# Kernel optimization log

Hardware: AMD Instinct MI355X
Metric: run time of the kernel (lower is better)

The kernel has to match this reference:

```python
import jax, jax.numpy as jnp
import numpy as np

N_BATCH, N_ATOMS = 32, 1024


def _param_tables():
    # Species ids: 0 = padding, 1 = H (Z=1), 2 = O (Z=8). Symmetric tables, pad row/col zero.
    d0 = np.zeros((3, 3), np.float32)
    p1 = np.zeros((3, 3), np.float32)
    p2 = np.zeros((3, 3), np.float32)
    d0[1, 1] = 157.5488; p1[1, 1] = -0.1661; p2[1, 1] = 6.25      # 001-001
    d0[1, 2] = d0[2, 1] = 216.7852                                 # 001-008
    p1[1, 2] = p1[2, 1] = -1.0
    p2[1, 2] = p2[2, 1] = 1.6492
    d0[2, 2] = 122.9794; p1[2, 2] = 1.0; p2[2, 2] = 0.1958         # 008-008
    return jnp.asarray(d0), jnp.asarray(p1), jnp.asarray(p2)


def setup_inputs() -> dict:
    key = jax.random.key(0)
    kz, kb = jax.random.split(key)
    # Atomic numbers in {1, 8} (H/O), the only species with params in the dict.
    zbits = jax.random.randint(kz, (N_BATCH, N_ATOMS), 0, 2)
    Z = jnp.where(zbits == 0, 1, 8).astype(jnp.int32)
    # Bond orders Pij in (0, 1); strictly positive so b**pbe2 is smooth.
    B = jax.random.uniform(kb, (N_BATCH, N_ATOMS, N_ATOMS), jnp.float32)
    d0_table, pbe1_table, pbe2_table = _param_tables()
    return {"Z": Z, "B": B, "d0_table": d0_table,
            "pbe1_table": pbe1_table, "pbe2_table": pbe2_table}


def reference(Z, B, d0_table, pbe1_table, pbe2_table):
    # Map atomic number -> table id (0 pad, 1 for Z=1, 2 for Z=8).
    zmap = jnp.zeros((9,), jnp.int32).at[1].set(1).at[8].set(2)
    idx = zmap[Z]                              # [nb, na]
    ii = idx[:, :, None]                       # species of atom i
    jj = idx[:, None, :]                       # species of atom j
    d0 = d0_table[ii, jj]                      # [nb, na, na] pairwise param gather
    p1 = pbe1_table[ii, jj]
    p2 = pbe2_table[ii, jj]
    # Original indexes B[:, jatom, iatom] for pair (i, j), i < j -> transpose.
    bij = jnp.abs(jnp.swapaxes(B, 1, 2))       # bij[b, i, j] = |B[b, j, i]|
    e_ij = -d0 * bij * jnp.exp(p1 * (1.0 - bij ** p2))
    n = Z.shape[1]
    pair_mask = jnp.triu(jnp.ones((n, n), bool), k=1)   # i < j only
    valid = pair_mask[None] & (Z[:, :, None] != 0) & (Z[:, None, :] != 0)
    E = jnp.sum(jnp.where(valid, e_ij, 0.0), axis=(1, 2))[:, None]  # [nb, 1]
    return E
```

## Files before the change

kernel.cpp:

```cpp
#include <hip/hip_runtime.h>

#define NATOMS  1024
#define NB      32
#define WPB     4
#define BLK     (WPB * 64)
#define BPBATCH 64
#define WAVES   (BPBATCH * WPB)
#define PPW     ((NATOMS / 2) / WAVES)

__global__ __launch_bounds__(BLK, 8) void reax_partial(
    const int*   __restrict__ Z,
    const float* __restrict__ B,
    const float* __restrict__ d0t,
    const float* __restrict__ p1t,
    const float* __restrict__ p2t,
    float*       __restrict__ ws)
{
    const int b    = blockIdx.y;
    const int wave = blockIdx.x * WPB + (threadIdx.x >> 6);
    const int lane = threadIdx.x & 63;

    const float LOG2E = 1.4426950408889634f;
    const float d0_0 = d0t[4], d0_1 = d0t[5], d0_2 = d0t[8];
    const float p1_0 = p1t[4], p1_1 = p1t[5], p1_2 = p1t[8];
    const float p2_0 = p2t[4], p2_1 = p2t[5], p2_2 = p2t[8];
    const float de_0 = d0_0 * __builtin_amdgcn_exp2f(p1_0 * LOG2E);
    const float de_1 = d0_1 * __builtin_amdgcn_exp2f(p1_1 * LOG2E);
    const float de_2 = d0_2 * __builtin_amdgcn_exp2f(p1_2 * LOG2E);
    const float c1_0 = -p1_0 * LOG2E, c1_1 = -p1_1 * LOG2E, c1_2 = -p1_2 * LOG2E;

    __shared__ float t_shf[NATOMS];
    const int* Zrow = Z + b * NATOMS;
    for (int i = threadIdx.x; i < NATOMS; i += BLK)
        t_shf[i] = (Zrow[i] == 8) ? 1.0f : 0.0f;
    __syncthreads();

    const float* Bb = B + (size_t)b * NATOMS * NATOMS;
    float sum0 = 0.0f, sum1 = 0.0f;

    for (int pp = 0; pp < PPW; ++pp) {
        const int p = wave + pp * WAVES;
        #pragma unroll
        for (int r = 0; r < 2; ++r) {
            const int j = r ? (NATOMS - 1 - p) : p;
            if (j == 0) continue;
            const int tj = (t_shf[j] != 0.0f);
            const float dea = tj ? de_1 : de_0, dde = tj ? (de_2 - de_1) : (de_1 - de_0);
            const float c1a = tj ? c1_1 : c1_0, dc1 = tj ? (c1_2 - c1_1) : (c1_1 - c1_0);
            const float p2a = tj ? p2_1 : p2_0, dp2 = tj ? (p2_2 - p2_1) : (p2_1 - p2_0);

            const float*  Brow  = Bb + (size_t)j * NATOMS;
            const float4* Brow4 = (const float4*)Brow;
            const float4* Trow4 = (const float4*)t_shf;
            const int nv = j >> 2;

            #define ELEM(xc, tc, acc)                                       \
            {                                                               \
                const float bb  = fabsf(xc);                                \
                const float p2  = fmaf(tc, dp2, p2a);                       \
                const float c1  = fmaf(tc, dc1, c1a);                       \
                const float de  = fmaf(tc, dde, dea);                       \
                const float lg  = __builtin_amdgcn_logf(bb);                \
                const float pw  = __builtin_amdgcn_exp2f(p2 * lg);          \
                const float ex  = __builtin_amdgcn_exp2f(fmaf(c1, pw, lg)); \
                acc = fmaf(de, ex, acc);                                    \
            }

            #pragma unroll 4
            for (int v = lane; v < nv; v += 64) {
                const float4 x  = Brow4[v];
                const float4 t4 = Trow4[v];
                ELEM(x.x, t4.x, sum0) ELEM(x.y, t4.y, sum1)
                ELEM(x.z, t4.z, sum0) ELEM(x.w, t4.w, sum1)
            }
            const int i = (nv << 2) + lane;
            if (i < j) {
                ELEM(Brow[i], t_shf[i], sum0)
            }
            #undef ELEM
        }
    }

    float sum = sum0 + sum1;
    #pragma unroll
    for (int off = 32; off; off >>= 1) sum += __shfl_down(sum, off, 64);
    if (lane == 0) ws[b * WAVES + wave] = sum;
}

__global__ __launch_bounds__(64) void reax_reduce(
    const float* __restrict__ ws, float* __restrict__ out)
{
    const int b = blockIdx.x;
    const int t = threadIdx.x;
    float s = ws[b * WAVES + t]       + ws[b * WAVES + t + 64]
            + ws[b * WAVES + t + 128] + ws[b * WAVES + t + 192];
    #pragma unroll
    for (int off = 32; off; off >>= 1) s += __shfl_down(s, off, 64);
    if (t == 0) out[b] = -s;
}

extern "C" void kernel_launch(void* const* d_in, const int* in_sizes, int n_in,
                              void* d_out, int out_size, void* d_ws, size_t ws_size,
                              hipStream_t stream) {
    const int*   Z   = (const int*)  d_in[0];
    const float* B   = (const float*)d_in[1];
    const float* d0t = (const float*)d_in[2];
    const float* p1t = (const float*)d_in[3];
    const float* p2t = (const float*)d_in[4];
    float* out = (float*)d_out;
    float* ws  = (float*)d_ws;

    dim3 grid(BPBATCH, NB);
    reax_partial<<<grid, BLK, 0, stream>>>(Z, B, d0t, p1t, p2t, ws);
    reax_reduce<<<NB, 64, 0, stream>>>(ws, out);
}
```

Measured before the change: 23.79 us.

## Fuse reduction into main kernel via atomics and register-cache species row

Removes the second reduction kernel: each block sums its wave partials in shared memory and atomically adds into the output, which is zeroed with a memset beforehand. The species flags for the whole row are loaded once into four float4 registers per lane, replacing per-iteration shared-memory loads, and the inner loop is fully unrolled into four guarded steps. It also drops the occupancy hint from launch bounds. The cost is a memset launch, float atomics with nondeterministic summation order, and higher register pressure.

```diff
diff --git a/kernel.cpp b/kernel.cpp
--- a/kernel.cpp
+++ b/kernel.cpp
@@ -8,13 +8,13 @@
 #define WAVES   (BPBATCH * WPB)
 #define PPW     ((NATOMS / 2) / WAVES)
 
-__global__ __launch_bounds__(BLK, 8) void reax_partial(
+__global__ __launch_bounds__(BLK) void reax_fused(
     const int*   __restrict__ Z,
     const float* __restrict__ B,
     const float* __restrict__ d0t,
     const float* __restrict__ p1t,
     const float* __restrict__ p2t,
-    float*       __restrict__ ws)
+    float*       __restrict__ out)
 {
     const int b    = blockIdx.y;
     const int wave = blockIdx.x * WPB + (threadIdx.x >> 6);
@@ -35,6 +35,12 @@
         t_shf[i] = (Zrow[i] == 8) ? 1.0f : 0.0f;
     __syncthreads();
 
+    const float4* Trow4 = (const float4*)t_shf;
+    const float4 tt0 = Trow4[lane];
+    const float4 tt1 = Trow4[lane + 64];
+    const float4 tt2 = Trow4[lane + 128];
+    const float4 tt3 = Trow4[lane + 192];
+
     const float* Bb = B + (size_t)b * NATOMS * NATOMS;
     float sum0 = 0.0f, sum1 = 0.0f;
 
@@ -51,7 +57,6 @@
 
             const float*  Brow  = Bb + (size_t)j * NATOMS;
             const float4* Brow4 = (const float4*)Brow;
-            const float4* Trow4 = (const float4*)t_shf;
             const int nv = j >> 2;
 
             #define ELEM(xc, tc, acc)                                       \
@@ -66,13 +71,18 @@
                 acc = fmaf(de, ex, acc);                                    \
             }
 
-            #pragma unroll 4
-            for (int v = lane; v < nv; v += 64) {
-                const float4 x  = Brow4[v];
-                const float4 t4 = Trow4[v];
-                ELEM(x.x, t4.x, sum0) ELEM(x.y, t4.y, sum1)
-                ELEM(x.z, t4.z, sum0) ELEM(x.w, t4.w, sum1)
+            #define KSTEP(K, TT)                                            \
+            {                                                               \
+                const int v = lane + 64 * (K);                              \
+                if (v < nv) {                                               \
+                    const float4 x = Brow4[v];                              \
+                    ELEM(x.x, TT.x, sum0) ELEM(x.y, TT.y, sum1)             \
+                    ELEM(x.z, TT.z, sum0) ELEM(x.w, TT.w, sum1)             \
+                }                                                           \
             }
+            KSTEP(0, tt0) KSTEP(1, tt1) KSTEP(2, tt2) KSTEP(3, tt3)
+            #undef KSTEP
+
             const int i = (nv << 2) + lane;
             if (i < j) {
                 ELEM(Brow[i], t_shf[i], sum0)
@@ -84,19 +94,14 @@
     float sum = sum0 + sum1;
     #pragma unroll
     for (int off = 32; off; off >>= 1) sum += __shfl_down(sum, off, 64);
-    if (lane == 0) ws[b * WAVES + wave] = sum;
-}
 
-__global__ __launch_bounds__(64) void reax_reduce(
-    const float* __restrict__ ws, float* __restrict__ out)
-{
-    const int b = blockIdx.x;
-    const int t = threadIdx.x;
-    float s = ws[b * WAVES + t]       + ws[b * WAVES + t + 64]
-            + ws[b * WAVES + t + 128] + ws[b * WAVES + t + 192];
-    #pragma unroll
-    for (int off = 32; off; off >>= 1) s += __shfl_down(s, off, 64);
-    if (t == 0) out[b] = -s;
+    __shared__ float wsum[WPB];
+    if (lane == 0) wsum[threadIdx.x >> 6] = sum;
+    __syncthreads();
+    if (threadIdx.x == 0) {
+        const float block_sum = wsum[0] + wsum[1] + wsum[2] + wsum[3];
+        atomicAdd(&out[b], -block_sum);
+    }
 }
 
 extern "C" void kernel_launch(void* const* d_in, const int* in_sizes, int n_in,
@@ -108,9 +113,8 @@
     const float* p1t = (const float*)d_in[3];
     const float* p2t = (const float*)d_in[4];
     float* out = (float*)d_out;
-    float* ws  = (float*)d_ws;
 
+    hipMemsetAsync(out, 0, NB * sizeof(float), stream);
     dim3 grid(BPBATCH, NB);
-    reax_partial<<<grid, BLK, 0, stream>>>(Z, B, d0t, p1t, p2t, ws);
-    reax_reduce<<<NB, 64, 0, stream>>>(ws, out);
+    reax_fused<<<grid, BLK, 0, stream>>>(Z, B, d0t, p1t, p2t, out);
 }
```

After: 39.31 us. +65.2%, slower.
